# Kernel optimization log

Hardware: AMD Instinct MI355X
Metric: run time of the kernel (lower is better)

The kernel has to match this reference:

```python
import jax, jax.numpy as jnp
import numpy as np


def setup_inputs() -> dict:
    key = jax.random.key(0)
    ks = jax.random.split(key, 8)
    B = 32768
    return {
        "x": jax.random.normal(ks[0], (B, 784), dtype=jnp.float32),
        "conv_w": jax.random.normal(ks[1], (3, 3), dtype=jnp.float32),
        "fc1_w": jax.random.normal(ks[2], (512, 676), dtype=jnp.float32) * 0.04,
        "fc1_b": jax.random.normal(ks[3], (512,), dtype=jnp.float32),
        "fc2_w": jax.random.normal(ks[4], (512, 512), dtype=jnp.float32) * 0.04,
        "fc2_b": jax.random.normal(ks[5], (512,), dtype=jnp.float32),
        "out_w": jax.random.normal(ks[6], (10, 512), dtype=jnp.float32) * 0.04,
        "out_b": jax.random.normal(ks[7], (10,), dtype=jnp.float32),
    }


def reference(x, conv_w, fc1_w, fc1_b, fc2_w, fc2_b, out_w, out_b):
    B = x.shape[0]
    img = x.reshape(B, 1, 28, 28)  # NCHW, single channel
    # Valid 3x3 cross-correlation (same math as the nested tensordot loop).
    kern = conv_w.reshape(1, 1, 3, 3)  # OIHW
    conv = jax.lax.conv_general_dilated(
        img, kern, window_strides=(1, 1), padding="VALID",
        dimension_numbers=("NCHW", "OIHW", "NCHW"))  # [B,1,26,26]
    h = conv.reshape(B, 26 * 26)
    h = jax.nn.relu(h @ fc1_w.T + fc1_b)
    h = jax.nn.relu(h @ fc2_w.T + fc2_b)
    return h @ out_w.T + out_b  # [B,10] logits
```

## Files before the change

### kernel.cpp

```cpp
#include <hip/hip_runtime.h>

typedef unsigned short ushort_t;
typedef __attribute__((ext_vector_type(8))) short bf16x8;
typedef __attribute__((ext_vector_type(4))) float f32x4;
typedef __attribute__((ext_vector_type(4))) unsigned short u16x4;
typedef __attribute__((ext_vector_type(16))) float f32x16;

__device__ __forceinline__ unsigned short f2bf(float f) {
    union { float f; unsigned u; } v; v.f = f;
    unsigned r = v.u + 0x7FFFu + ((v.u >> 16) & 1u);
    return (unsigned short)(r >> 16);
}

__device__ __forceinline__ unsigned cvt_pk_bf16(float a, float b) {
    unsigned r;
    asm("v_cvt_pk_bf16_f32 %0, %1, %2" : "=v"(r) : "v"(a), "v"(b));
    return r;
}

__global__ __launch_bounds__(256) void prep_w(const float* __restrict__ fc1_w,
                                              const float* __restrict__ cw,
                                              const float* __restrict__ fc2_w,
                                              const float* __restrict__ out_w,
                                              ushort_t* __restrict__ W1,
                                              ushort_t* __restrict__ W2,
                                              ushort_t* __restrict__ W3) {
    __shared__ float Fp[4][900];
    const int tid = threadIdx.x, bid = blockIdx.x;
    if (bid < 128) {
        const int wid = tid >> 6, lane = tid & 63;
        const int n = bid * 4 + wid;
        float* F = Fp[wid];
#pragma unroll
        for (int t = 0; t < 15; ++t) {
            const int i = t * 64 + lane;
            if (i < 900) F[i] = 0.f;
        }
        __syncthreads();
#pragma unroll
        for (int t = 0; t < 11; ++t) {
            const int i = t * 64 + lane;
            if (i < 676) {
                const int r = i / 26, c = i - r * 26;
                F[(r + 2) * 30 + (c + 2)] = fc1_w[n * 676 + i];
            }
        }
        __syncthreads();
        const float k00 = cw[0], k01 = cw[1], k02 = cw[2];
        const float k10 = cw[3], k11 = cw[4], k12 = cw[5];
        const float k20 = cw[6], k21 = cw[7], k22 = cw[8];
        const int ngrp = n >> 5, r32n = n & 31;
#pragma unroll
        for (int t = 0; t < 13; ++t) {
            const int p = t * 64 + lane;
            float v = 0.f;
            if (p < 784) {
                const int pr = p / 28, pc = p - pr * 28;
                const int rb = (pr + 2) * 30 + (pc + 2);
                v = k00 * F[rb]      + k01 * F[rb - 1]  + k02 * F[rb - 2]
                  + k10 * F[rb - 30] + k11 * F[rb - 31] + k12 * F[rb - 32]
                  + k20 * F[rb - 60] + k21 * F[rb - 61] + k22 * F[rb - 62];
            }
            W1[(ngrp * 52 + (p >> 4)) * 512 + (((p >> 3) & 1) * 32 + r32n) * 8 + (p & 7)] = f2bf(v);
        }
    } else if (bid < 384) {
        const int base = (bid - 128) * 1024 + tid * 4;
        const int ngrp = base >> 14;
        const int kfrag = (base >> 9) & 31;
        const int li = base & 511;
        const int lane = li >> 3;
        const int n = ngrp * 32 + (lane & 31);
        const int p0 = kfrag * 16 + (lane >> 5) * 8 + (li & 7);
        const f32x4 v = *(const f32x4*)&fc2_w[n * 512 + p0];
        u16x4 o;
        o[0] = f2bf(v.x); o[1] = f2bf(v.y); o[2] = f2bf(v.z); o[3] = f2bf(v.w);
        *(u16x4*)&W2[base] = o;
    } else {
        for (int idx = tid; idx < 8192; idx += 256)
            W3[idx] = (idx < 5120) ? f2bf(out_w[idx]) : (ushort_t)0;
    }
}

__global__ __launch_bounds__(512, 4) void mega13(const float* __restrict__ x,
                                                 const ushort_t* __restrict__ W1,
                                                 const ushort_t* __restrict__ W2,
                                                 const ushort_t* __restrict__ W3,
                                                 const float* __restrict__ b1,
                                                 const float* __restrict__ b2,
                                                 const float* __restrict__ ob,
                                                 float* __restrict__ out) {
    extern __shared__ ushort_t smem[];
    ushort_t* xs0 = smem;
    ushort_t* hs  = smem + 4096;

    const int tid = threadIdx.x;
    const int wave = tid >> 6, lane = tid & 63;
    const int r32 = lane & 31, khalf = lane >> 5;
    const int xrow = tid >> 3, xoct = tid & 7;
    const int m0 = blockIdx.x * 64;
    const size_t ng0 = wave * 2, ng1 = wave * 2 + 1;

    const ushort_t* w1p0 = &W1[ng0 * 52 * 512 + lane * 8];
    const ushort_t* w1p1 = &W1[ng1 * 52 * 512 + lane * 8];
    const ushort_t* w2p0 = &W2[ng0 * 32 * 512 + lane * 8];
    const ushort_t* w2p1 = &W2[ng1 * 32 * 512 + lane * 8];

    f32x16 acc[2][2];
#pragma unroll
    for (int a = 0; a < 2; ++a)
#pragma unroll
        for (int j = 0; j < 2; ++j)
#pragma unroll
            for (int e = 0; e < 16; ++e) acc[a][j][e] = 0.f;

    f32x4 xv0, xv1;
    auto load_x = [&](int ks) {
        const int gc = ks * 64 + xoct * 8;
        if (gc < 784) {
            const f32x4* p = (const f32x4*)&x[(size_t)(m0 + xrow) * 784 + gc];
            xv0 = __builtin_nontemporal_load(p);
            xv1 = __builtin_nontemporal_load(p + 1);
        } else {
            xv0 = (f32x4){0.f, 0.f, 0.f, 0.f};
            xv1 = (f32x4){0.f, 0.f, 0.f, 0.f};
        }
    };
    auto store_x = [&](ushort_t* buf) {
        union { bf16x8 h; unsigned u[4]; } a;
        a.u[0] = cvt_pk_bf16(xv0.x, xv0.y); a.u[1] = cvt_pk_bf16(xv0.z, xv0.w);
        a.u[2] = cvt_pk_bf16(xv1.x, xv1.y); a.u[3] = cvt_pk_bf16(xv1.z, xv1.w);
        *(bf16x8*)&buf[xrow * 64 + ((xoct ^ (xrow & 7)) * 8)] = a.h;
    };

    auto write_h = [&](const float* __restrict__ bias) {
#pragma unroll
        for (int j = 0; j < 2; ++j) {
            const int n = (wave * 2 + j) * 32 + r32;
            const float bb = bias[n];
            const int nseg = n >> 3, nrem = n & 7;
#pragma unroll
            for (int i = 0; i < 2; ++i)
#pragma unroll
                for (int reg = 0; reg < 16; ++reg) {
                    const int m = i * 32 + 4 * khalf + (reg & 3) + 8 * (reg >> 2);
                    hs[m * 512 + ((nseg ^ (m & 7)) * 8) + nrem] = f2bf(fmaxf(acc[i][j][reg] + bb, 0.f));
                }
        }
    };

    load_x(0);
    store_x(xs0);
    __syncthreads();

    bf16x8 bwc0 = *(const bf16x8*)(w1p0);
    bf16x8 bwc1 = *(const bf16x8*)(w1p1);

    for (int ks = 0; ks < 12; ++ks) {
        load_x(ks + 1);
        const ushort_t* bufp = (ks & 1) ? hs : xs0;
#pragma unroll
        for (int ksub = 0; ksub < 4; ++ksub) {
            const int kf = ks * 4 + ksub;
            bf16x8 bwn0, bwn1;
            if (kf < 48) {
                bwn0 = *(const bf16x8*)(w1p0 + (kf + 1) * 512);
                bwn1 = *(const bf16x8*)(w1p1 + (kf + 1) * 512);
            } else {
                bwn0 = *(const bf16x8*)(w2p0);
                bwn1 = *(const bf16x8*)(w2p1);
            }
            const int q = 2 * ksub + khalf;
            bf16x8 af[2];
#pragma unroll
            for (int i = 0; i < 2; ++i) {
                const int m = i * 32 + r32;
                af[i] = *(const bf16x8*)&bufp[m * 64 + ((q ^ (m & 7)) * 8)];
            }
            __builtin_amdgcn_s_setprio(1);
            acc[0][0] = __builtin_amdgcn_mfma_f32_32x32x16_bf16(af[0], bwc0, acc[0][0], 0, 0, 0);
            acc[0][1] = __builtin_amdgcn_mfma_f32_32x32x16_bf16(af[0], bwc1, acc[0][1], 0, 0, 0);
            acc[1][0] = __builtin_amdgcn_mfma_f32_32x32x16_bf16(af[1], bwc0, acc[1][0], 0, 0, 0);
            acc[1][1] = __builtin_amdgcn_mfma_f32_32x32x16_bf16(af[1], bwc1, acc[1][1], 0, 0, 0);
            __builtin_amdgcn_s_setprio(0);
            bwc0 = bwn0; bwc1 = bwn1;
        }
        store_x((ks & 1) ? xs0 : hs);
        __syncthreads();
    }
    {
        const ushort_t* bufp = xs0;
        bf16x8 bwn0 = *(const bf16x8*)(w2p0);
        bf16x8 bwn1 = *(const bf16x8*)(w2p1);
        const int q = khalf;
        bf16x8 af[2];
#pragma unroll
        for (int i = 0; i < 2; ++i) {
            const int m = i * 32 + r32;
            af[i] = *(const bf16x8*)&bufp[m * 64 + ((q ^ (m & 7)) * 8)];
        }
        __builtin_amdgcn_s_setprio(1);
        acc[0][0] = __builtin_amdgcn_mfma_f32_32x32x16_bf16(af[0], bwc0, acc[0][0], 0, 0, 0);
        acc[0][1] = __builtin_amdgcn_mfma_f32_32x32x16_bf16(af[0], bwc1, acc[0][1], 0, 0, 0);
        acc[1][0] = __builtin_amdgcn_mfma_f32_32x32x16_bf16(af[1], bwc0, acc[1][0], 0, 0, 0);
        acc[1][1] = __builtin_amdgcn_mfma_f32_32x32x16_bf16(af[1], bwc1, acc[1][1], 0, 0, 0);
        __builtin_amdgcn_s_setprio(0);
        bwc0 = bwn0; bwc1 = bwn1;
    }

    write_h(b1);
#pragma unroll
    for (int a = 0; a < 2; ++a)
#pragma unroll
        for (int j = 0; j < 2; ++j)
#pragma unroll
            for (int e = 0; e < 16; ++e) acc[a][j][e] = 0.f;
    __syncthreads();

    for (int ks = 0; ks < 8; ++ks) {
#pragma unroll
        for (int ksub = 0; ksub < 4; ++ksub) {
            const int kf = ks * 4 + ksub;
            bf16x8 bwn0, bwn1;
            if (kf < 31) {
                bwn0 = *(const bf16x8*)(w2p0 + (kf + 1) * 512);
                bwn1 = *(const bf16x8*)(w2p1 + (kf + 1) * 512);
            }
            const int hq = kf * 2 + khalf;
            bf16x8 af[2];
#pragma unroll
            for (int i = 0; i < 2; ++i) {
                const int m = i * 32 + r32;
                af[i] = *(const bf16x8*)&hs[m * 512 + ((hq ^ (m & 7)) * 8)];
            }
            __builtin_amdgcn_s_setprio(1);
            acc[0][0] = __builtin_amdgcn_mfma_f32_32x32x16_bf16(af[0], bwc0, acc[0][0], 0, 0, 0);
            acc[0][1] = __builtin_amdgcn_mfma_f32_32x32x16_bf16(af[0], bwc1, acc[0][1], 0, 0, 0);
            acc[1][0] = __builtin_amdgcn_mfma_f32_32x32x16_bf16(af[1], bwc0, acc[1][0], 0, 0, 0);
            acc[1][1] = __builtin_amdgcn_mfma_f32_32x32x16_bf16(af[1], bwc1, acc[1][1], 0, 0, 0);
            __builtin_amdgcn_s_setprio(0);
            if (kf < 31) { bwc0 = bwn0; bwc1 = bwn1; }
        }
    }
    __syncthreads();

    write_h(b2);
    __syncthreads();

    if (wave < 4) {
        const int quad = lane >> 4, l16 = lane & 15;
        const int row = wave * 16 + l16;
        f32x4 hacc = {0.f, 0.f, 0.f, 0.f};
#pragma unroll
        for (int ks = 0; ks < 16; ++ks) {
            const int seg = 4 * ks + quad;
            const bf16x8 a = *(const bf16x8*)&hs[row * 512 + ((seg ^ (row & 7)) * 8)];
            const bf16x8 b = *(const bf16x8*)&W3[l16 * 512 + ks * 32 + quad * 8];
            hacc = __builtin_amdgcn_mfma_f32_16x16x32_bf16(a, b, hacc, 0, 0, 0);
        }
        if (l16 < 10) {
            const float bb = ob[l16];
#pragma unroll
            for (int r = 0; r < 4; ++r)
                out[(size_t)(m0 + wave * 16 + quad * 4 + r) * 10 + l16] = hacc[r] + bb;
        }
    }
}

extern "C" void kernel_launch(void* const* d_in, const int* in_sizes, int n_in,
                              void* d_out, int out_size, void* d_ws, size_t ws_size,
                              hipStream_t stream) {
    const float* x      = (const float*)d_in[0];
    const float* conv_w = (const float*)d_in[1];
    const float* fc1_w  = (const float*)d_in[2];
    const float* fc1_b  = (const float*)d_in[3];
    const float* fc2_w  = (const float*)d_in[4];
    const float* fc2_b  = (const float*)d_in[5];
    const float* out_w  = (const float*)d_in[6];
    const float* out_b  = (const float*)d_in[7];
    float* out = (float*)d_out;

    ushort_t* W1 = (ushort_t*)d_ws;
    ushort_t* W2 = W1 + 425984;
    ushort_t* W3 = W2 + 262144;

    prep_w<<<dim3(385), 256, 0, stream>>>(fc1_w, conv_w, fc2_w, out_w, W1, W2, W3);

    mega13<<<dim3(512), 512, 73728, stream>>>(x, W1, W2, W3, fc1_b, fc2_b, out_b, out);
}
```

Measured before the change: 220.8 us.

## Double K-step width for x staging, stagger weight fragments per wave, drop register prefetch

```diff
diff --git a/kernel.cpp b/kernel.cpp
--- a/kernel.cpp
+++ b/kernel.cpp
@@ -81,7 +81,7 @@
     }
 }
 
-__global__ __launch_bounds__(512, 4) void mega13(const float* __restrict__ x,
+__global__ __launch_bounds__(512, 4) void mega16(const float* __restrict__ x,
                                                  const ushort_t* __restrict__ W1,
                                                  const ushort_t* __restrict__ W2,
                                                  const ushort_t* __restrict__ W3,
@@ -90,8 +90,9 @@
                                                  const float* __restrict__ ob,
                                                  float* __restrict__ out) {
     extern __shared__ ushort_t smem[];
-    ushort_t* xs0 = smem;
-    ushort_t* hs  = smem + 4096;
+    ushort_t* hs = smem;
+    ushort_t* xbA = smem;
+    ushort_t* xbB = smem + 8192;
 
     const int tid = threadIdx.x;
     const int wave = tid >> 6, lane = tid & 63;
@@ -113,23 +114,24 @@
 #pragma unroll
             for (int e = 0; e < 16; ++e) acc[a][j][e] = 0.f;
 
-    f32x4 xv0, xv1;
+    f32x4 xv0, xv1, xv2, xv3;
     auto load_x = [&](int ks) {
-        const int gc = ks * 64 + xoct * 8;
-        if (gc < 784) {
-            const f32x4* p = (const f32x4*)&x[(size_t)(m0 + xrow) * 784 + gc];
-            xv0 = __builtin_nontemporal_load(p);
-            xv1 = __builtin_nontemporal_load(p + 1);
-        } else {
-            xv0 = (f32x4){0.f, 0.f, 0.f, 0.f};
-            xv1 = (f32x4){0.f, 0.f, 0.f, 0.f};
-        }
+        const int gc0 = ks * 128 + xoct * 16;
+        const float* p = &x[(size_t)(m0 + xrow) * 784 + gc0];
+        xv0 = (gc0      < 784) ? __builtin_nontemporal_load((const f32x4*)p)       : (f32x4){0.f,0.f,0.f,0.f};
+        xv1 = (gc0 + 4  < 784) ? __builtin_nontemporal_load((const f32x4*)(p + 4)) : (f32x4){0.f,0.f,0.f,0.f};
+        xv2 = (gc0 + 8  < 784) ? __builtin_nontemporal_load((const f32x4*)(p + 8)) : (f32x4){0.f,0.f,0.f,0.f};
+        xv3 = (gc0 + 12 < 784) ? __builtin_nontemporal_load((const f32x4*)(p + 12)): (f32x4){0.f,0.f,0.f,0.f};
     };
     auto store_x = [&](ushort_t* buf) {
-        union { bf16x8 h; unsigned u[4]; } a;
+        union { bf16x8 h; unsigned u[4]; } a, b;
         a.u[0] = cvt_pk_bf16(xv0.x, xv0.y); a.u[1] = cvt_pk_bf16(xv0.z, xv0.w);
         a.u[2] = cvt_pk_bf16(xv1.x, xv1.y); a.u[3] = cvt_pk_bf16(xv1.z, xv1.w);
-        *(bf16x8*)&buf[xrow * 64 + ((xoct ^ (xrow & 7)) * 8)] = a.h;
+        b.u[0] = cvt_pk_bf16(xv2.x, xv2.y); b.u[1] = cvt_pk_bf16(xv2.z, xv2.w);
+        b.u[2] = cvt_pk_bf16(xv3.x, xv3.y); b.u[3] = cvt_pk_bf16(xv3.z, xv3.w);
+        const int s0 = xoct * 2, sw = xrow & 7;
+        *(bf16x8*)&buf[xrow * 128 + (((s0    ) ^ sw) * 8)] = a.h;
+        *(bf16x8*)&buf[xrow * 128 + (((s0 + 1) ^ sw) * 8)] = b.h;
     };
 
     auto write_h = [&](const float* __restrict__ bias) {
@@ -149,63 +151,54 @@
     };
 
     load_x(0);
-    store_x(xs0);
-    __syncthreads();
-
-    bf16x8 bwc0 = *(const bf16x8*)(w1p0);
-    bf16x8 bwc1 = *(const bf16x8*)(w1p1);
-
-    for (int ks = 0; ks < 12; ++ks) {
+    store_x(xbA);
+    __syncthreads();
+
+    for (int ks = 0; ks < 6; ++ks) {
         load_x(ks + 1);
-        const ushort_t* bufp = (ks & 1) ? hs : xs0;
-#pragma unroll
-        for (int ksub = 0; ksub < 4; ++ksub) {
-            const int kf = ks * 4 + ksub;
-            bf16x8 bwn0, bwn1;
-            if (kf < 48) {
-                bwn0 = *(const bf16x8*)(w1p0 + (kf + 1) * 512);
-                bwn1 = *(const bf16x8*)(w1p1 + (kf + 1) * 512);
-            } else {
-                bwn0 = *(const bf16x8*)(w2p0);
-                bwn1 = *(const bf16x8*)(w2p1);
-            }
-            const int q = 2 * ksub + khalf;
+        const ushort_t* bufp = (ks & 1) ? xbB : xbA;
+#pragma unroll
+        for (int ksub = 0; ksub < 8; ++ksub) {
+            const int kq = (ksub + wave) & 7;
+            const int kf = ks * 8 + kq;
+            const bf16x8 bw0 = *(const bf16x8*)(w1p0 + (size_t)kf * 512);
+            const bf16x8 bw1 = *(const bf16x8*)(w1p1 + (size_t)kf * 512);
+            const int q = 2 * kq + khalf;
             bf16x8 af[2];
 #pragma unroll
             for (int i = 0; i < 2; ++i) {
                 const int m = i * 32 + r32;
-                af[i] = *(const bf16x8*)&bufp[m * 64 + ((q ^ (m & 7)) * 8)];
+                af[i] = *(const bf16x8*)&bufp[m * 128 + ((q ^ (m & 7)) * 8)];
             }
             __builtin_amdgcn_s_setprio(1);
-            acc[0][0] = __builtin_amdgcn_mfma_f32_32x32x16_bf16(af[0], bwc0, acc[0][0], 0, 0, 0);
-            acc[0][1] = __builtin_amdgcn_mfma_f32_32x32x16_bf16(af[0], bwc1, acc[0][1], 0, 0, 0);
-            acc[1][0] = __builtin_amdgcn_mfma_f32_32x32x16_bf16(af[1], bwc0, acc[1][0], 0, 0, 0);
-            acc[1][1] = __builtin_amdgcn_mfma_f32_32x32x16_bf16(af[1], bwc1, acc[1][1], 0, 0, 0);
+            acc[0][0] = __builtin_amdgcn_mfma_f32_32x32x16_bf16(af[0], bw0, acc[0][0], 0, 0, 0);
+            acc[0][1] = __builtin_amdgcn_mfma_f32_32x32x16_bf16(af[0], bw1, acc[0][1], 0, 0, 0);
+            acc[1][0] = __builtin_amdgcn_mfma_f32_32x32x16_bf16(af[1], bw0, acc[1][0], 0, 0, 0);
+            acc[1][1] = __builtin_amdgcn_mfma_f32_32x32x16_bf16(af[1], bw1, acc[1][1], 0, 0, 0);
             __builtin_amdgcn_s_setprio(0);
-            bwc0 = bwn0; bwc1 = bwn1;
-        }
-        store_x((ks & 1) ? xs0 : hs);
+        }
+        store_x((ks & 1) ? xbA : xbB);
         __syncthreads();
     }
     {
-        const ushort_t* bufp = xs0;
-        bf16x8 bwn0 = *(const bf16x8*)(w2p0);
-        bf16x8 bwn1 = *(const bf16x8*)(w2p1);
+        const ushort_t* bufp = xbA;
+        const bf16x8 bw0 = *(const bf16x8*)(w1p0 + (size_t)48 * 512);
+        const bf16x8 bw1 = *(const bf16x8*)(w1p1 + (size_t)48 * 512);
         const int q = khalf;
         bf16x8 af[2];
 #pragma unroll
         for (int i = 0; i < 2; ++i) {
             const int m = i * 32 + r32;
-            af[i] = *(const bf16x8*)&bufp[m * 64 + ((q ^ (m & 7)) * 8)];
+            af[i] = *(const bf16x8*)&bufp[m * 128 + ((q ^ (m & 7)) * 8)];
         }
         __builtin_amdgcn_s_setprio(1);
-        acc[0][0] = __builtin_amdgcn_mfma_f32_32x32x16_bf16(af[0], bwc0, acc[0][0], 0, 0, 0);
-        acc[0][1] = __builtin_amdgcn_mfma_f32_32x32x16_bf16(af[0], bwc1, acc[0][1], 0, 0, 0);
-        acc[1][0] = __builtin_amdgcn_mfma_f32_32x32x16_bf16(af[1], bwc0, acc[1][0], 0, 0, 0);
-        acc[1][1] = __builtin_amdgcn_mfma_f32_32x32x16_bf16(af[1], bwc1, acc[1][1], 0, 0, 0);
+        acc[0][0] = __builtin_amdgcn_mfma_f32_32x32x16_bf16(af[0], bw0, acc[0][0], 0, 0, 0);
+        acc[0][1] = __builtin_amdgcn_mfma_f32_32x32x16_bf16(af[0], bw1, acc[0][1], 0, 0, 0);
+        acc[1][0] = __builtin_amdgcn_mfma_f32_32x32x16_bf16(af[1], bw0, acc[1][0], 0, 0, 0);
+        acc[1][1] = __builtin_amdgcn_mfma_f32_32x32x16_bf16(af[1], bw1, acc[1][1], 0, 0, 0);
         __builtin_amdgcn_s_setprio(0);
-        bwc0 = bwn0; bwc1 = bwn1;
-    }
+    }
+    __syncthreads();
 
     write_h(b1);
 #pragma unroll
@@ -216,15 +209,13 @@
             for (int e = 0; e < 16; ++e) acc[a][j][e] = 0.f;
     __syncthreads();
 
-    for (int ks = 0; ks < 8; ++ks) {
-#pragma unroll
-        for (int ksub = 0; ksub < 4; ++ksub) {
-            const int kf = ks * 4 + ksub;
-            bf16x8 bwn0, bwn1;
-            if (kf < 31) {
-                bwn0 = *(const bf16x8*)(w2p0 + (kf + 1) * 512);
-                bwn1 = *(const bf16x8*)(w2p1 + (kf + 1) * 512);
-            }
+    for (int ks2 = 0; ks2 < 4; ++ks2) {
+#pragma unroll
+        for (int ksub = 0; ksub < 8; ++ksub) {
+            const int kq = (ksub + wave) & 7;
+            const int kf = ks2 * 8 + kq;
+            const bf16x8 bw0 = *(const bf16x8*)(w2p0 + (size_t)kf * 512);
+            const bf16x8 bw1 = *(const bf16x8*)(w2p1 + (size_t)kf * 512);
             const int hq = kf * 2 + khalf;
             bf16x8 af[2];
 #pragma unroll
@@ -233,12 +224,11 @@
                 af[i] = *(const bf16x8*)&hs[m * 512 + ((hq ^ (m & 7)) * 8)];
             }
             __builtin_amdgcn_s_setprio(1);
-            acc[0][0] = __builtin_amdgcn_mfma_f32_32x32x16_bf16(af[0], bwc0, acc[0][0], 0, 0, 0);
-            acc[0][1] = __builtin_amdgcn_mfma_f32_32x32x16_bf16(af[0], bwc1, acc[0][1], 0, 0, 0);
-            acc[1][0] = __builtin_amdgcn_mfma_f32_32x32x16_bf16(af[1], bwc0, acc[1][0], 0, 0, 0);
-            acc[1][1] = __builtin_amdgcn_mfma_f32_32x32x16_bf16(af[1], bwc1, acc[1][1], 0, 0, 0);
+            acc[0][0] = __builtin_amdgcn_mfma_f32_32x32x16_bf16(af[0], bw0, acc[0][0], 0, 0, 0);
+            acc[0][1] = __builtin_amdgcn_mfma_f32_32x32x16_bf16(af[0], bw1, acc[0][1], 0, 0, 0);
+            acc[1][0] = __builtin_amdgcn_mfma_f32_32x32x16_bf16(af[1], bw0, acc[1][0], 0, 0, 0);
+            acc[1][1] = __builtin_amdgcn_mfma_f32_32x32x16_bf16(af[1], bw1, acc[1][1], 0, 0, 0);
             __builtin_amdgcn_s_setprio(0);
-            if (kf < 31) { bwc0 = bwn0; bwc1 = bwn1; }
         }
     }
     __syncthreads();
@@ -285,5 +275,5 @@
 
     prep_w<<<dim3(385), 256, 0, stream>>>(fc1_w, conv_w, fc2_w, out_w, W1, W2, W3);
 
-    mega13<<<dim3(512), 512, 73728, stream>>>(x, W1, W2, W3, fc1_b, fc2_b, out_b, out);
-}
+    mega16<<<dim3(512), 512, 65536, stream>>>(x, W1, W2, W3, fc1_b, fc2_b, out_b, out);
+}
```

Result: slower. 239.6 us (+8.5%).
